# Kernel tuning notes

Hardware: AMD Instinct MI355X
Metric: run time of the kernel (lower is better)

Reference implementation:

```python
import jax, jax.numpy as jnp
import numpy as np

NUM_BINS = 16
PADDING = 2.0


def _spline(u):
    # third-order (cubic B-spline) Parzen window kernel
    au = jnp.abs(u)
    su = au * au
    r1 = (4.0 - 6.0 * su + 3.0 * su * au) / 6.0          # |u| < 1
    r2 = (8.0 - 12.0 * au + 6.0 * su - su * au) / 6.0    # 1 <= |u| < 2
    return jnp.where(au < 1.0, r1, jnp.where(au < 2.0, r2, jnp.zeros_like(u)))


def setup_inputs() -> dict:
    key = jax.random.key(0)
    k1, k2 = jax.random.split(key)
    shape = (4, 1, 128, 128, 128)
    moving = jax.random.uniform(k1, shape, dtype=jnp.float32)
    fixed = jax.random.uniform(k2, shape, dtype=jnp.float32)
    return {"moving": moving, "fixed": fixed}


def reference(moving, fixed):
    nb = NUM_BINS
    B = moving.shape[0]
    m = moving.reshape(B, -1)
    f = fixed.reshape(B, -1)
    N = m.shape[1]

    fmin = f.min(1, keepdims=True); fmax = f.max(1, keepdims=True)
    mmin = m.min(1, keepdims=True); mmax = m.max(1, keepdims=True)
    fbs = (fmax - fmin) / (nb - 2.0 * PADDING)
    mbs = (mmax - mmin) / (nb - 2.0 * PADDING)

    # winTerm >= PADDING = 2, so int-truncation == floor
    f_term = f / fbs - (fmin / fbs - PADDING)
    m_term = m / mbs - (mmin / mbs - PADDING)
    f_idx = jnp.clip(f_term.astype(jnp.int32), 2, nb - 3)   # [B, N]
    m_idx = jnp.clip(m_term.astype(jnp.int32), 2, nb - 3)   # [B, N]

    b_off = jnp.arange(B, dtype=jnp.int32)[:, None]

    # joint histogram: 4-tap cubic spline scatter-add along the moving axis
    joint = jnp.zeros((B * nb * nb,), dtype=m.dtype)
    for off in (-1, 0, 1, 2):
        a = _spline((m_idx + off).astype(m_term.dtype) - m_term)  # [B, N]
        seg = (b_off * (nb * nb) + f_idx * nb + (m_idx + off)).ravel()
        joint = joint + jax.ops.segment_sum(a.ravel(), seg, num_segments=B * nb * nb)
    joint = joint.reshape(B, nb, nb)

    fixed_counts = jax.ops.segment_sum(
        jnp.ones((B * N,), dtype=m.dtype),
        (b_off * nb + f_idx).ravel(),
        num_segments=B * nb,
    ).reshape(B, nb)
    fixedPDF = fixed_counts / N                       # [B, nb]

    joint_norm = joint / joint.sum((1, 2), keepdims=True)   # [B, nb, nb]
    movingPDF = joint_norm.sum(1)                           # [B, nb]

    def plogp(p):
        return jnp.where(p > 0, p * jnp.log(jnp.where(p > 0, p, 1.0)), jnp.zeros_like(p))

    mi = plogp(joint_norm).sum((1, 2)) - plogp(movingPDF).sum(1) - plogp(fixedPDF).sum(1)
    return -jnp.mean(mi)
```

## Files before the change

### kernel.cpp

```cpp
#include <hip/hip_runtime.h>

#define NB 16
#define BATCHES 4
#define GX 128
#define BT 1024

typedef unsigned long long ull;

struct WS {
    float4 slot[BATCHES * GX];
    ull joint[BATCHES * 256];
    unsigned int ticket;
};


__global__ __launch_bounds__(BT) void k_minmax(const float4* __restrict__ mov,
                                               const float4* __restrict__ fix,
                                               WS* __restrict__ ws, int nvec) {
    int t = threadIdx.x;
    int b = blockIdx.y, bx = blockIdx.x;
    if (bx == 0 && b == 0) {
        ws->joint[t] = 0ull;
        if (t == 0) ws->ticket = 0u;
    }
    int q = nvec >> 9;
    const float4* fb = fix + (size_t)b * nvec + (size_t)bx * (nvec >> 7);
    const float4* mb = mov + (size_t)b * nvec + (size_t)bx * (nvec >> 7);
    float4 f0 = fb[t], f1 = fb[t + q], f2 = fb[t + 2 * q], f3 = fb[t + 3 * q];
    float4 m0 = mb[t], m1 = mb[t + q], m2 = mb[t + 2 * q], m3 = mb[t + 3 * q];

    float fmn = fminf(fminf(fminf(fminf(f0.x, f0.y), fminf(f0.z, f0.w)),
                            fminf(fminf(f1.x, f1.y), fminf(f1.z, f1.w))),
                      fminf(fminf(fminf(f2.x, f2.y), fminf(f2.z, f2.w)),
                            fminf(fminf(f3.x, f3.y), fminf(f3.z, f3.w))));
    float fmx = fmaxf(fmaxf(fmaxf(fmaxf(f0.x, f0.y), fmaxf(f0.z, f0.w)),
                            fmaxf(fmaxf(f1.x, f1.y), fmaxf(f1.z, f1.w))),
                      fmaxf(fmaxf(fmaxf(f2.x, f2.y), fmaxf(f2.z, f2.w)),
                            fmaxf(fmaxf(f3.x, f3.y), fmaxf(f3.z, f3.w))));
    float mmn = fminf(fminf(fminf(fminf(m0.x, m0.y), fminf(m0.z, m0.w)),
                            fminf(fminf(m1.x, m1.y), fminf(m1.z, m1.w))),
                      fminf(fminf(fminf(m2.x, m2.y), fminf(m2.z, m2.w)),
                            fminf(fminf(m3.x, m3.y), fminf(m3.z, m3.w))));
    float mmx = fmaxf(fmaxf(fmaxf(fmaxf(m0.x, m0.y), fmaxf(m0.z, m0.w)),
                            fmaxf(fmaxf(m1.x, m1.y), fmaxf(m1.z, m1.w))),
                      fmaxf(fmaxf(fmaxf(m2.x, m2.y), fmaxf(m2.z, m2.w)),
                            fmaxf(fmaxf(m3.x, m3.y), fmaxf(m3.z, m3.w))));

    for (int d = 32; d; d >>= 1) {
        fmn = fminf(fmn, __shfl_xor(fmn, d));
        fmx = fmaxf(fmx, __shfl_xor(fmx, d));
        mmn = fminf(mmn, __shfl_xor(mmn, d));
        mmx = fmaxf(mmx, __shfl_xor(mmx, d));
    }
    __shared__ float4 wred[16];
    int wid = t >> 6, lane = t & 63;
    if (lane == 0) wred[wid] = make_float4(fmn, fmx, mmn, mmx);
    __syncthreads();
    if (wid == 0) {
        float4 s = wred[lane & 15];
        for (int d = 8; d; d >>= 1) {
            s.x = fminf(s.x, __shfl_xor(s.x, d));
            s.y = fmaxf(s.y, __shfl_xor(s.y, d));
            s.z = fminf(s.z, __shfl_xor(s.z, d));
            s.w = fmaxf(s.w, __shfl_xor(s.w, d));
        }
        if (lane == 0) ws->slot[b * GX + bx] = s;
    }
}

__global__ __launch_bounds__(BT) void k_hist(const float4* __restrict__ mov,
                                             const float4* __restrict__ fix,
                                             WS* __restrict__ ws, int nvec,
                                             float* __restrict__ out) {
    __shared__ unsigned int ldsJ[16][256];
    __shared__ float4 mmbc;
    __shared__ bool isLast;
    __shared__ double shp[256];
    __shared__ double wsum[4];
    int t = threadIdx.x;
    int b = blockIdx.y, bx = blockIdx.x;
    int wid = t >> 6;

    #pragma unroll
    for (int i = 0; i < 4; i++) ((unsigned int*)ldsJ)[t + i * BT] = 0u;

    int q = nvec >> 9;
    const float4* fb = fix + (size_t)b * nvec + (size_t)bx * (nvec >> 7);
    const float4* mb = mov + (size_t)b * nvec + (size_t)bx * (nvec >> 7);
    float4 f0 = fb[t], f1 = fb[t + q], f2 = fb[t + 2 * q], f3 = fb[t + 3 * q];
    float4 m0 = mb[t], m1 = mb[t + q], m2 = mb[t + 2 * q], m3 = mb[t + 3 * q];

    if (t < 64) {
        float4 a = ws->slot[b * GX + t];
        float4 c = ws->slot[b * GX + t + 64];
        float4 s = make_float4(fminf(a.x, c.x), fmaxf(a.y, c.y),
                               fminf(a.z, c.z), fmaxf(a.w, c.w));
        for (int d = 32; d; d >>= 1) {
            s.x = fminf(s.x, __shfl_xor(s.x, d));
            s.y = fmaxf(s.y, __shfl_xor(s.y, d));
            s.z = fminf(s.z, __shfl_xor(s.z, d));
            s.w = fmaxf(s.w, __shfl_xor(s.w, d));
        }
        if (t == 0) mmbc = s;
    }
    __syncthreads();

    float fbs = (mmbc.y - mmbc.x) * (1.0f / 12.0f);
    float mbs = (mmbc.w - mmbc.z) * (1.0f / 12.0f);
    float finv = 1.0f / fbs;
    float minv = 1.0f / mbs;
    float fofs = __builtin_fmaf(-mmbc.x, finv, 2.0f);
    float mofs = __builtin_fmaf(-mmbc.z, minv, 2.0f);

    unsigned int* myJ = &ldsJ[wid][0];

    auto proc = [&](float fv, float mv) {
        float fterm = __builtin_fmaf(fv, finv, fofs);
        int fi = (int)fterm;
        fi = fi < 2 ? 2 : (fi > NB - 3 ? NB - 3 : fi);
        float mterm = __builtin_fmaf(mv, minv, mofs);
        int mi_ = (int)mterm;
        mi_ = mi_ < 2 ? 2 : (mi_ > NB - 3 ? NB - 3 : mi_);
        float tt = fminf(fmaxf(mterm - (float)mi_, 0.0f), 1.0f);
        float t2 = tt * tt;
        float omt = 1.0f - tt;
        float w0 = omt * omt * omt * (1.0f / 6.0f);
        float w3 = tt * t2 * (1.0f / 6.0f);
        float w1 = __builtin_fmaf(__builtin_fmaf(3.0f, tt, -6.0f), t2, 4.0f) * (1.0f / 6.0f);
        float w2 = fmaxf(1.0f - w0 - w1 - w3, 0.0f);
        int row = fi << 4;
        int s0 = (mi_ - 1 + 5 * fi) & 15;
        atomicAdd(myJ + row + s0,              (unsigned int)(w0 * 2097152.0f));
        atomicAdd(myJ + row + ((s0 + 1) & 15), (unsigned int)(w1 * 2097152.0f));
        atomicAdd(myJ + row + ((s0 + 2) & 15), (unsigned int)(w2 * 2097152.0f));
        atomicAdd(myJ + row + ((s0 + 3) & 15), (unsigned int)(w3 * 2097152.0f));
    };

    proc(f0.x, m0.x); proc(f0.y, m0.y); proc(f0.z, m0.z); proc(f0.w, m0.w);
    proc(f1.x, m1.x); proc(f1.y, m1.y); proc(f1.z, m1.z); proc(f1.w, m1.w);
    proc(f2.x, m2.x); proc(f2.y, m2.y); proc(f2.z, m2.z); proc(f2.w, m2.w);
    proc(f3.x, m3.x); proc(f3.y, m3.y); proc(f3.z, m3.z); proc(f3.w, m3.w);
    __syncthreads();

    if (t < 256) {
        ull v = 0;
        #pragma unroll
        for (int c = 0; c < 16; c++) v += (ull)ldsJ[c][t];
        if (v) atomicAdd(&ws->joint[b * 256 + t], v);
    }

    if (t == 0) {
        __threadfence();
        unsigned int done = atomicAdd(&ws->ticket, 1u);
        isLast = (done == (unsigned int)(gridDim.x * gridDim.y) - 1u);
    }
    __syncthreads();
    if (!isLast) return;

    double acc = 0.0;
    for (int bb = 0; bb < BATCHES; ++bb) {
        double v = 0.0;
        ull qq = 0ull;
        if (t < 256) {
            qq = atomicAdd(&ws->joint[bb * 256 + t], 0ull);
            v = (double)qq;
        }
        double s = v;
        for (int d = 32; d; d >>= 1) s += __shfl_xor(s, d);
        if (t < 256 && (t & 63) == 0) wsum[t >> 6] = s;
        __syncthreads();
        double total = wsum[0] + wsum[1] + wsum[2] + wsum[3];
        double p = (t < 256) ? v / total : 0.0;
        int f = t >> 4, c = t & 15, m = (c - 5 * f) & 15;
        if (t < 256) shp[f * 16 + m] = p;
        double val = (t < 256 && qq != 0ull) ? p * log(p) : 0.0;
        __syncthreads();
        if (t < 16) {
            double mp = 0.0;
            #pragma unroll
            for (int f2 = 0; f2 < 16; ++f2) mp += shp[f2 * 16 + t];
            if (mp > 0.0) val -= mp * log(mp);
        } else if (t < 32) {
            int f2 = t - 16;
            double fp = 0.0;
            #pragma unroll
            for (int m2 = 0; m2 < 16; ++m2) fp += shp[f2 * 16 + m2];
            if (fp > 0.0) val -= fp * log(fp);
        }
        double s2 = val;
        for (int d = 32; d; d >>= 1) s2 += __shfl_xor(s2, d);
        __syncthreads();
        if (t < 256 && (t & 63) == 0) wsum[t >> 6] = s2;
        __syncthreads();
        if (t == 0) acc += wsum[0] + wsum[1] + wsum[2] + wsum[3];
        __syncthreads();
    }
    if (t == 0) out[0] = (float)(-acc / (double)BATCHES);
}

extern "C" void kernel_launch(void* const* d_in, const int* in_sizes, int n_in,
                              void* d_out, int out_size, void* d_ws, size_t ws_size,
                              hipStream_t stream) {
    const float* mov = (const float*)d_in[0];
    const float* fix = (const float*)d_in[1];
    float* out = (float*)d_out;
    WS* ws = (WS*)d_ws;

    int total = in_sizes[0];
    int N = total / BATCHES;
    int nvec = N / 4;

    dim3 grid(GX, BATCHES);
    k_minmax<<<grid, BT, 0, stream>>>((const float4*)mov, (const float4*)fix, ws, nvec);
    k_hist<<<grid, BT, 0, stream>>>((const float4*)mov, (const float4*)fix, ws, nvec, out);
}
```

Baseline: 120.3 us.

## Fuse min/max and histogram kernels with a grid-wide spin barrier

Merges the two launches into one persistent kernel of 256 blocks. Each block computes its local min/max, then all blocks wait on a global atomic ticket barrier gated by a magic ready flag before building the histogram. Each block now covers twice as many elements, reloading them from global memory after the barrier. This removes a kernel launch and the gap between launches. In exchange, it depends on all 256 blocks being co-resident, otherwise the spin barrier deadlocks, and it re-reads the inputs, which will likely be L2 hits.

Result: slower. 123.8 us (+2.9%).

```diff
diff --git a/kernel.cpp b/kernel.cpp
--- a/kernel.cpp
+++ b/kernel.cpp
@@ -2,99 +2,93 @@
 
 #define NB 16
 #define BATCHES 4
-#define GX 128
+#define GXB 64
 #define BT 1024
+#define MAGIC 0x7F3A9C51u
 
 typedef unsigned long long ull;
 
 struct WS {
-    float4 slot[BATCHES * GX];
+    unsigned int ready;
+    unsigned int ticket;
+    unsigned int ticket2;
+    unsigned int hdrpad[29];
+    float4 slot[BATCHES * GXB];
     ull joint[BATCHES * 256];
-    unsigned int ticket;
 };
 
-
-__global__ __launch_bounds__(BT) void k_minmax(const float4* __restrict__ mov,
-                                               const float4* __restrict__ fix,
-                                               WS* __restrict__ ws, int nvec) {
+__global__ __launch_bounds__(BT, 8) void k_mi(const float4* __restrict__ mov,
+                                              const float4* __restrict__ fix,
+                                              WS* __restrict__ ws, int nvec,
+                                              float* __restrict__ out) {
+    __shared__ unsigned int ldsJ[16][256];
+    __shared__ float4 wred[16];
+    __shared__ float4 mmbc;
+    __shared__ bool isLast;
+    __shared__ double shp[256];
+    __shared__ double wsum[4];
+
     int t = threadIdx.x;
     int b = blockIdx.y, bx = blockIdx.x;
-    if (bx == 0 && b == 0) {
-        ws->joint[t] = 0ull;
-        if (t == 0) ws->ticket = 0u;
-    }
-    int q = nvec >> 9;
-    const float4* fb = fix + (size_t)b * nvec + (size_t)bx * (nvec >> 7);
-    const float4* mb = mov + (size_t)b * nvec + (size_t)bx * (nvec >> 7);
-    float4 f0 = fb[t], f1 = fb[t + q], f2 = fb[t + 2 * q], f3 = fb[t + 3 * q];
-    float4 m0 = mb[t], m1 = mb[t + q], m2 = mb[t + 2 * q], m3 = mb[t + 3 * q];
-
-    float fmn = fminf(fminf(fminf(fminf(f0.x, f0.y), fminf(f0.z, f0.w)),
-                            fminf(fminf(f1.x, f1.y), fminf(f1.z, f1.w))),
-                      fminf(fminf(fminf(f2.x, f2.y), fminf(f2.z, f2.w)),
-                            fminf(fminf(f3.x, f3.y), fminf(f3.z, f3.w))));
-    float fmx = fmaxf(fmaxf(fmaxf(fmaxf(f0.x, f0.y), fmaxf(f0.z, f0.w)),
-                            fmaxf(fmaxf(f1.x, f1.y), fmaxf(f1.z, f1.w))),
-                      fmaxf(fmaxf(fmaxf(f2.x, f2.y), fmaxf(f2.z, f2.w)),
-                            fmaxf(fmaxf(f3.x, f3.y), fmaxf(f3.z, f3.w))));
-    float mmn = fminf(fminf(fminf(fminf(m0.x, m0.y), fminf(m0.z, m0.w)),
-                            fminf(fminf(m1.x, m1.y), fminf(m1.z, m1.w))),
-                      fminf(fminf(fminf(m2.x, m2.y), fminf(m2.z, m2.w)),
-                            fminf(fminf(m3.x, m3.y), fminf(m3.z, m3.w))));
-    float mmx = fmaxf(fmaxf(fmaxf(fmaxf(m0.x, m0.y), fmaxf(m0.z, m0.w)),
-                            fmaxf(fmaxf(m1.x, m1.y), fmaxf(m1.z, m1.w))),
-                      fmaxf(fmaxf(fmaxf(m2.x, m2.y), fmaxf(m2.z, m2.w)),
-                            fmaxf(fmaxf(m3.x, m3.y), fmaxf(m3.z, m3.w))));
-
+    int wid = t >> 6, lane = t & 63;
+    unsigned int nblk = gridDim.x * gridDim.y;
+
+    if (b == 0 && bx == 0) ws->joint[t] = 0ull;
+
+    #pragma unroll
+    for (int i = 0; i < 4; i++) ((unsigned int*)ldsJ)[t + i * BT] = 0u;
+
+    int slice = nvec / GXB;
+    const float4* fb = fix + (size_t)b * nvec + (size_t)bx * slice;
+    const float4* mb = mov + (size_t)b * nvec + (size_t)bx * slice;
+
+    float fmn = 3.4e38f, fmx = -3.4e38f, mmn = 3.4e38f, mmx = -3.4e38f;
+    #pragma unroll
+    for (int k = 0; k < 8; k += 2) {
+        float4 a = fb[t + k * BT], c = fb[t + (k + 1) * BT];
+        float4 d = mb[t + k * BT], e = mb[t + (k + 1) * BT];
+        fmn = fminf(fmn, fminf(fminf(fminf(a.x, a.y), fminf(a.z, a.w)),
+                               fminf(fminf(c.x, c.y), fminf(c.z, c.w))));
+        fmx = fmaxf(fmx, fmaxf(fmaxf(fmaxf(a.x, a.y), fmaxf(a.z, a.w)),
+                               fmaxf(fmaxf(c.x, c.y), fmaxf(c.z, c.w))));
+        mmn = fminf(mmn, fminf(fminf(fminf(d.x, d.y), fminf(d.z, d.w)),
+                               fminf(fminf(e.x, e.y), fminf(e.z, e.w))));
+        mmx = fmaxf(mmx, fmaxf(fmaxf(fmaxf(d.x, d.y), fmaxf(d.z, d.w)),
+                               fmaxf(fmaxf(e.x, e.y), fmaxf(e.z, e.w))));
+    }
     for (int d = 32; d; d >>= 1) {
         fmn = fminf(fmn, __shfl_xor(fmn, d));
         fmx = fmaxf(fmx, __shfl_xor(fmx, d));
         mmn = fminf(mmn, __shfl_xor(mmn, d));
         mmx = fmaxf(mmx, __shfl_xor(mmx, d));
     }
-    __shared__ float4 wred[16];
-    int wid = t >> 6, lane = t & 63;
     if (lane == 0) wred[wid] = make_float4(fmn, fmx, mmn, mmx);
     __syncthreads();
-    if (wid == 0) {
-        float4 s = wred[lane & 15];
-        for (int d = 8; d; d >>= 1) {
-            s.x = fminf(s.x, __shfl_xor(s.x, d));
-            s.y = fmaxf(s.y, __shfl_xor(s.y, d));
-            s.z = fminf(s.z, __shfl_xor(s.z, d));
-            s.w = fmaxf(s.w, __shfl_xor(s.w, d));
-        }
-        if (lane == 0) ws->slot[b * GX + bx] = s;
-    }
-}
-
-__global__ __launch_bounds__(BT) void k_hist(const float4* __restrict__ mov,
-                                             const float4* __restrict__ fix,
-                                             WS* __restrict__ ws, int nvec,
-                                             float* __restrict__ out) {
-    __shared__ unsigned int ldsJ[16][256];
-    __shared__ float4 mmbc;
-    __shared__ bool isLast;
-    __shared__ double shp[256];
-    __shared__ double wsum[4];
-    int t = threadIdx.x;
-    int b = blockIdx.y, bx = blockIdx.x;
-    int wid = t >> 6;
-
-    #pragma unroll
-    for (int i = 0; i < 4; i++) ((unsigned int*)ldsJ)[t + i * BT] = 0u;
-
-    int q = nvec >> 9;
-    const float4* fb = fix + (size_t)b * nvec + (size_t)bx * (nvec >> 7);
-    const float4* mb = mov + (size_t)b * nvec + (size_t)bx * (nvec >> 7);
-    float4 f0 = fb[t], f1 = fb[t + q], f2 = fb[t + 2 * q], f3 = fb[t + 3 * q];
-    float4 m0 = mb[t], m1 = mb[t + q], m2 = mb[t + 2 * q], m3 = mb[t + 3 * q];
+
+    if (t == 0) {
+        float4 s = wred[0];
+        #pragma unroll
+        for (int w = 1; w < 16; w++) {
+            float4 a = wred[w];
+            s.x = fminf(s.x, a.x); s.y = fmaxf(s.y, a.y);
+            s.z = fminf(s.z, a.z); s.w = fmaxf(s.w, a.w);
+        }
+        ws->slot[b * GXB + bx] = s;
+        __threadfence();
+        if (b == 0 && bx == 0) {
+            atomicExch(&ws->ticket, 0u);
+            atomicExch(&ws->ticket2, 0u);
+            __threadfence();
+            atomicExch(&ws->ready, MAGIC);
+        }
+        while (atomicAdd(&ws->ready, 0u) != MAGIC) __builtin_amdgcn_s_sleep(8);
+        atomicAdd(&ws->ticket, 1u);
+        while (atomicAdd(&ws->ticket, 0u) < nblk) __builtin_amdgcn_s_sleep(8);
+    }
+    __syncthreads();
 
     if (t < 64) {
-        float4 a = ws->slot[b * GX + t];
-        float4 c = ws->slot[b * GX + t + 64];
-        float4 s = make_float4(fminf(a.x, c.x), fmaxf(a.y, c.y),
-                               fminf(a.z, c.z), fmaxf(a.w, c.w));
+        float4 s = ws->slot[b * GXB + lane];
         for (int d = 32; d; d >>= 1) {
             s.x = fminf(s.x, __shfl_xor(s.x, d));
             s.y = fmaxf(s.y, __shfl_xor(s.y, d));
@@ -136,10 +130,13 @@
         atomicAdd(myJ + row + ((s0 + 3) & 15), (unsigned int)(w3 * 2097152.0f));
     };
 
-    proc(f0.x, m0.x); proc(f0.y, m0.y); proc(f0.z, m0.z); proc(f0.w, m0.w);
-    proc(f1.x, m1.x); proc(f1.y, m1.y); proc(f1.z, m1.z); proc(f1.w, m1.w);
-    proc(f2.x, m2.x); proc(f2.y, m2.y); proc(f2.z, m2.z); proc(f2.w, m2.w);
-    proc(f3.x, m3.x); proc(f3.y, m3.y); proc(f3.z, m3.z); proc(f3.w, m3.w);
+    #pragma unroll
+    for (int k = 0; k < 8; k += 2) {
+        float4 fA = fb[t + k * BT], fB = fb[t + (k + 1) * BT];
+        float4 mA = mb[t + k * BT], mB = mb[t + (k + 1) * BT];
+        proc(fA.x, mA.x); proc(fA.y, mA.y); proc(fA.z, mA.z); proc(fA.w, mA.w);
+        proc(fB.x, mB.x); proc(fB.y, mB.y); proc(fB.z, mB.z); proc(fB.w, mB.w);
+    }
     __syncthreads();
 
     if (t < 256) {
@@ -151,8 +148,8 @@
 
     if (t == 0) {
         __threadfence();
-        unsigned int done = atomicAdd(&ws->ticket, 1u);
-        isLast = (done == (unsigned int)(gridDim.x * gridDim.y) - 1u);
+        unsigned int done = atomicAdd(&ws->ticket2, 1u);
+        isLast = (done == nblk - 1u);
     }
     __syncthreads();
     if (!isLast) return;
@@ -195,7 +192,11 @@
         if (t == 0) acc += wsum[0] + wsum[1] + wsum[2] + wsum[3];
         __syncthreads();
     }
-    if (t == 0) out[0] = (float)(-acc / (double)BATCHES);
+    if (t == 0) {
+        out[0] = (float)(-acc / (double)BATCHES);
+        __threadfence();
+        atomicExch(&ws->ready, 0u);
+    }
 }
 
 extern "C" void kernel_launch(void* const* d_in, const int* in_sizes, int n_in,
@@ -210,7 +211,6 @@
     int N = total / BATCHES;
     int nvec = N / 4;
 
-    dim3 grid(GX, BATCHES);
-    k_minmax<<<grid, BT, 0, stream>>>((const float4*)mov, (const float4*)fix, ws, nvec);
-    k_hist<<<grid, BT, 0, stream>>>((const float4*)mov, (const float4*)fix, ws, nvec, out);
+    dim3 grid(GXB, BATCHES);
+    k_mi<<<grid, BT, 0, stream>>>((const float4*)mov, (const float4*)fix, ws, nvec, out);
 }
```
